# Kernel tuning notes

Measured on AMD Instinct MI355X. Metric: run time of the kernel, lower is better.

The kernel has to match this reference:

```python
import jax, jax.numpy as jnp
import numpy as np

KLD_SCALE = 10.0
COMMITMENT_COST = 0.1


def setup_inputs() -> dict:
    key = jax.random.key(0)
    k1, k2 = jax.random.split(key)
    z = jax.random.normal(k1, (32, 2048, 64), dtype=jnp.float32)
    codebook = jax.random.normal(k2, (1024, 64), dtype=jnp.float32)
    return {"z": z, "codebook": codebook}


def reference(z, codebook):
    B, N, D = z.shape
    z_e = z.reshape(B * N, D)                          # (M, D)
    # squared euclidean distance: ||z||^2 - 2 z.E^T + ||E||^2
    dist = (
        jnp.sum(z_e * z_e, axis=1, keepdims=True)
        - 2.0 * (z_e @ codebook.T)
        + jnp.sum(codebook * codebook, axis=1)[None, :]
    )                                                  # (M, K)
    ind = jnp.argmin(dist, axis=1)                     # (M,)
    z_q = codebook[ind]                                # (M, D) gather
    latent_loss = (
        COMMITMENT_COST * jnp.mean((jax.lax.stop_gradient(z_q) - z_e) ** 2)
        + jnp.mean((z_q - jax.lax.stop_gradient(z_e)) ** 2)
    ) * KLD_SCALE
    # straight-through estimator
    z_q_st = z_e + jax.lax.stop_gradient(z_q - z_e)
    return z_q_st.reshape(B, N, D), latent_loss
```

## Files before the change

### kernel.cpp

```cpp
#include <hip/hip_runtime.h>
#include <hip/hip_bf16.h>
#include <float.h>

#define DIMS 64
#define KC 1024
#define M_TOTAL 65536
#define TAU 4e-3f

typedef __attribute__((ext_vector_type(8))) short bf16x8;
typedef __attribute__((ext_vector_type(4))) float f32x4;

#define SE_OFF   0
#define CTL_OFF  1024
#define PART_OFF 2048
#define PBH_OFF  4096
#define PBL_OFF  36864
#define IDX_OFF  69632
#define WL_OFF   135168

#define WBAR(N) asm volatile("s_waitcnt vmcnt(" #N ")\n\ts_barrier" ::: "memory")

__device__ inline short f2bf(float x) {
  union { __hip_bfloat16 h; short s; } u;
  u.h = __float2bfloat16(x);
  return u.s;
}
__device__ inline float bf2f(short x) {
  union { short s; __hip_bfloat16 h; } u;
  u.s = x;
  return __bfloat162float(u.h);
}

__device__ inline void gload_lds16(const void* g, void* l) {
  __builtin_amdgcn_global_load_lds(
      (const __attribute__((address_space(1))) void*)g,
      (__attribute__((address_space(3))) void*)l, 16, 0, 0);
}

__global__ __launch_bounds__(256) void k_prep(const float* __restrict__ cb,
                                              float* __restrict__ se,
                                              unsigned int* __restrict__ ctl,
                                              unsigned short* __restrict__ pbh,
                                              unsigned short* __restrict__ pbl) {
  const int tid = blockIdx.x * 256 + threadIdx.x;
  if (tid < 4) ctl[tid] = 0;
  const int l = tid & 63;
  const int s = (tid >> 6) & 1;
  const int tt = tid >> 7;
  const int code = tt * 16 + (l & 15);
  const int k = s * 32 + (l >> 4) * 8;
  const float* p = cb + (size_t)code * DIMS + k;
  float v[8];
  ((float4*)v)[0] = ((const float4*)p)[0];
  ((float4*)v)[1] = ((const float4*)p)[1];
  bf16x8 h, lo;
#pragma unroll
  for (int j = 0; j < 8; ++j) {
    short hj = f2bf(v[j]);
    h[j] = hj;
    lo[j] = f2bf(v[j] - bf2f(hj));
  }
  *(bf16x8*)(pbh + (size_t)tid * 8) = h;
  *(bf16x8*)(pbl + (size_t)tid * 8) = lo;

  if (tid < KC) {
    const float4* q = (const float4*)(cb + (size_t)tid * DIMS);
    float a0 = 0.f, a1 = 0.f, a2 = 0.f, a3 = 0.f;
#pragma unroll
    for (int i = 0; i < DIMS / 4; ++i) {
      float4 u = q[i];
      a0 = fmaf(u.x, u.x, a0);
      a1 = fmaf(u.y, u.y, a1);
      a2 = fmaf(u.z, u.z, a2);
      a3 = fmaf(u.w, u.w, a3);
    }
    se[tid] = (a0 + a1) + (a2 + a3);
  }
}

__device__ inline void loadA(const float* zp, bf16x8& h, bf16x8& lo) {
  float v[8];
  ((float4*)v)[0] = ((const float4*)zp)[0];
  ((float4*)v)[1] = ((const float4*)zp)[1];
#pragma unroll
  for (int j = 0; j < 8; ++j) {
    float s = -2.f * v[j];
    short hj = f2bf(s);
    h[j] = hj;
    lo[j] = f2bf(s - bf2f(hj));
  }
}

#define UPD(dv, m1v, m2v, btv)                        \
  {                                                   \
    float d_ = (dv);                                  \
    m2v = __builtin_amdgcn_fmed3f(d_, m1v, m2v);      \
    bool lt_ = d_ < m1v;                              \
    m1v = lt_ ? d_ : m1v;                             \
    btv = lt_ ? ct : btv;                             \
  }

__global__ __launch_bounds__(256, 4) void k_dist(const float* __restrict__ z,
                                                 const unsigned short* __restrict__ pbh,
                                                 const unsigned short* __restrict__ pbl,
                                                 const float* __restrict__ se,
                                                 int* __restrict__ idxo,
                                                 int* __restrict__ wl,
                                                 unsigned int* __restrict__ ctl) {
  __shared__ bf16x8 sB[3][2][256];
  __shared__ float sSE[KC];
  const int l = threadIdx.x & 63;
  const int w = threadIdx.x >> 6;
  const int r0 = blockIdx.x * 64 + w * 16;
  const int col = l & 15;
  const int g = l >> 4;

  const float* zp = z + (size_t)(r0 + col) * DIMS + g * 8;
  bf16x8 ah0, ah1, al0, al1;
  loadA(zp, ah0, al0);
  loadA(zp + 32, ah1, al1);

  gload_lds16(se + w * 256 + l * 4, &sSE[w * 256]);
  {
    const size_t f0 = (size_t)w * 64 + l;
    gload_lds16(pbh + f0 * 8, &sB[0][0][w * 64]);
    gload_lds16(pbl + f0 * 8, &sB[0][1][w * 64]);
    const size_t f1 = 256 + (size_t)w * 64 + l;
    gload_lds16(pbh + f1 * 8, &sB[1][0][w * 64]);
    gload_lds16(pbl + f1 * 8, &sB[1][1][w * 64]);
  }

  float m10 = FLT_MAX, m11 = FLT_MAX, m12 = FLT_MAX, m13 = FLT_MAX;
  float m20 = FLT_MAX, m21 = FLT_MAX, m22 = FLT_MAX, m23 = FLT_MAX;
  int bt0 = 0, bt1 = 0, bt2 = 0, bt3 = 0;

  int bufc = 0;
  for (int c = 0; c < 32; ++c) {
    if (c == 31) {
      WBAR(0);
    } else {
      WBAR(2);
    }
#pragma unroll
    for (int tt = 0; tt < 2; ++tt) {
      const int ct = c * 2 + tt;
      bf16x8 bh0 = sB[bufc][0][tt * 128 + l];
      bf16x8 bh1 = sB[bufc][0][tt * 128 + 64 + l];
      bf16x8 bl0 = sB[bufc][1][tt * 128 + l];
      bf16x8 bl1 = sB[bufc][1][tt * 128 + 64 + l];
      const float sec = sSE[ct * 16 + col];
      f32x4 acc = {sec, sec, sec, sec};
      __builtin_amdgcn_s_setprio(1);
      acc = __builtin_amdgcn_mfma_f32_16x16x32_bf16(ah0, bh0, acc, 0, 0, 0);
      acc = __builtin_amdgcn_mfma_f32_16x16x32_bf16(ah1, bh1, acc, 0, 0, 0);
      acc = __builtin_amdgcn_mfma_f32_16x16x32_bf16(ah0, bl0, acc, 0, 0, 0);
      acc = __builtin_amdgcn_mfma_f32_16x16x32_bf16(ah1, bl1, acc, 0, 0, 0);
      acc = __builtin_amdgcn_mfma_f32_16x16x32_bf16(al0, bh0, acc, 0, 0, 0);
      acc = __builtin_amdgcn_mfma_f32_16x16x32_bf16(al1, bh1, acc, 0, 0, 0);
      __builtin_amdgcn_s_setprio(0);
      UPD(acc[0], m10, m20, bt0);
      UPD(acc[1], m11, m21, bt1);
      UPD(acc[2], m12, m22, bt2);
      UPD(acc[3], m13, m23, bt3);
    }
    if (c < 30) {
      int nb = bufc + 2;
      if (nb >= 3) nb -= 3;
      const size_t f = (size_t)(c + 2) * 256 + w * 64 + l;
      gload_lds16(pbh + f * 8, &sB[nb][0][w * 64]);
      gload_lds16(pbl + f * 8, &sB[nb][1][w * 64]);
    }
    bufc++;
    if (bufc == 3) bufc = 0;
  }

  float m1s[4] = {m10, m11, m12, m13};
  float m2s[4] = {m20, m21, m22, m23};
  int bts[4] = {bt0, bt1, bt2, bt3};
#pragma unroll
  for (int j = 0; j < 4; ++j) {
    float m1j = m1s[j], m2j = m2s[j];
    int ij = bts[j] * 16 + col;
    for (int msk = 1; msk <= 8; msk <<= 1) {
      float o1 = __shfl_xor(m1j, msk);
      float o2 = __shfl_xor(m2j, msk);
      int oi = __shfl_xor(ij, msk);
      bool take = (o1 < m1j) || (o1 == m1j && oi < ij);
      float hi = take ? m1j : o1;
      m2j = fminf(fminf(m2j, o2), hi);
      m1j = take ? o1 : m1j;
      ij = take ? oi : ij;
    }
    if (col == 0) {
      const int row = r0 + g * 4 + j;
      idxo[row] = ij;
      if (m2j - m1j < TAU) {
        int p = atomicAdd((int*)ctl, 1);
        wl[p] = row;
      }
    }
  }
}

__global__ __launch_bounds__(256) void k_refine(const float* __restrict__ z,
                                                const float* __restrict__ cb,
                                                const int* __restrict__ wl,
                                                const unsigned int* __restrict__ ctl,
                                                int* __restrict__ idxo) {
  __shared__ float zz[64];
  __shared__ double sd[256];
  __shared__ int si[256];
  const int t = threadIdx.x;
  const int n = (int)ctl[0];
  for (int wi = blockIdx.x; wi < n; wi += 512) {
    const int row = wl[wi];
    if (t < 16) ((float4*)zz)[t] = ((const float4*)(z + (size_t)row * DIMS))[t];
    __syncthreads();
    const int c0 = t * 4;
    double accd[4] = {0.0, 0.0, 0.0, 0.0};
    for (int ch = 0; ch < 4; ++ch) {
      float zr[16];
#pragma unroll
      for (int q = 0; q < 4; ++q) ((float4*)zr)[q] = ((float4*)zz)[ch * 4 + q];
#pragma unroll
      for (int cc = 0; cc < 4; ++cc) {
        const float* e = cb + (size_t)(c0 + cc) * DIMS + ch * 16;
#pragma unroll
        for (int q = 0; q < 16; ++q) {
          double df = (double)zr[q] - (double)e[q];
          accd[cc] = fma(df, df, accd[cc]);
        }
      }
    }
    double best = 1e300;
    int bi = 0;
#pragma unroll
    for (int cc = 0; cc < 4; ++cc)
      if (accd[cc] < best) { best = accd[cc]; bi = c0 + cc; }
    sd[t] = best;
    si[t] = bi;
    __syncthreads();
    for (int off = 128; off > 0; off >>= 1) {
      if (t < off) {
        double ob = sd[t + off];
        int oi = si[t + off];
        if (ob < sd[t] || (ob == sd[t] && oi < si[t])) { sd[t] = ob; si[t] = oi; }
      }
      __syncthreads();
    }
    if (t == 0) idxo[row] = si[0];
    __syncthreads();
  }
}

__global__ __launch_bounds__(256) void k_out(const float* __restrict__ z,
                                             const float* __restrict__ cb,
                                             const int* __restrict__ idxi,
                                             float* __restrict__ out,
                                             float* __restrict__ partials) {
  const int tid = blockIdx.x * 256 + threadIdx.x;
  const int row = tid >> 2;
  const int q = tid & 3;
  const int code = idxi[row];
  const float4* zp = (const float4*)(z + (size_t)row * DIMS + q * 16);
  const float4* ep = (const float4*)(cb + (size_t)code * DIMS + q * 16);
  float4* op = (float4*)(out + (size_t)row * DIMS + q * 16);
  float sse = 0.f;
#pragma unroll
  for (int i = 0; i < 4; ++i) {
    float4 v = zp[i], e = ep[i];
    float dx = e.x - v.x, dy = e.y - v.y, dz = e.z - v.z, dw = e.w - v.w;
    sse = fmaf(dx, dx, sse);
    sse = fmaf(dy, dy, sse);
    sse = fmaf(dz, dz, sse);
    sse = fmaf(dw, dw, sse);
    float4 o;
    o.x = v.x + dx;
    o.y = v.y + dy;
    o.z = v.z + dz;
    o.w = v.w + dw;
    op[i] = o;
  }
  __shared__ float sh[256];
  sh[threadIdx.x] = sse;
  __syncthreads();
  for (int off = 128; off > 0; off >>= 1) {
    if (threadIdx.x < off) sh[threadIdx.x] += sh[threadIdx.x + off];
    __syncthreads();
  }
  if (threadIdx.x == 0) partials[blockIdx.x] = sh[0];
}

__global__ __launch_bounds__(256) void k_loss(const float* __restrict__ partials,
                                              float* __restrict__ out) {
  __shared__ float sh[256];
  const int t = threadIdx.x;
  sh[t] = partials[t] + partials[t + 256] + partials[t + 512] + partials[t + 768];
  __syncthreads();
  for (int off = 128; off > 0; off >>= 1) {
    if (t < off) sh[t] += sh[t + off];
    __syncthreads();
  }
  if (t == 0) {
    out[(size_t)M_TOTAL * DIMS] = sh[0] * (11.0f / (float)((size_t)M_TOTAL * DIMS));
  }
}

extern "C" void kernel_launch(void* const* d_in, const int* in_sizes, int n_in,
                              void* d_out, int out_size, void* d_ws, size_t ws_size,
                              hipStream_t stream) {
  const float* z = (const float*)d_in[0];
  const float* cb = (const float*)d_in[1];
  float* out = (float*)d_out;
  float* ws = (float*)d_ws;

  float* se = ws + SE_OFF;
  unsigned int* ctl = (unsigned int*)(ws + CTL_OFF);
  float* partials = ws + PART_OFF;
  unsigned short* pbh = (unsigned short*)(ws + PBH_OFF);
  unsigned short* pbl = (unsigned short*)(ws + PBL_OFF);
  int* idx = (int*)(ws + IDX_OFF);
  int* wl = (int*)(ws + WL_OFF);

  k_prep<<<32, 256, 0, stream>>>(cb, se, ctl, pbh, pbl);
  k_dist<<<M_TOTAL / 64, 256, 0, stream>>>(z, pbh, pbl, se, idx, wl, ctl);
  k_refine<<<512, 256, 0, stream>>>(z, cb, wl, ctl, idx);
  k_out<<<M_TOTAL / 64, 256, 0, stream>>>(z, cb, idx, out, partials);
  k_loss<<<1, 256, 0, stream>>>(partials, out);
}
```

Measured before the change: 58.64 us.

## Switch codebook staging to double buffer with syncthreads and read norms from global

Replaces the triple-buffered async LDS pipeline (two chunks in flight, explicit vmcnt waits) with a simpler double buffer that prefetches one chunk ahead and uses __syncthreads each iteration. The codebook-norm array is no longer staged in LDS and is read directly from global memory per tile, and the MFMA priority hints are removed. This lowers LDS usage and may raise occupancy. In exchange it shortens prefetch depth, relies on __syncthreads to drain the LDS-targeted loads, and adds global loads inside the inner loop.

Result: slower. 60.09 us (+2.5%).

```diff
diff --git a/kernel.cpp b/kernel.cpp
--- a/kernel.cpp
+++ b/kernel.cpp
@@ -17,8 +17,6 @@
 #define PBL_OFF  36864
 #define IDX_OFF  69632
 #define WL_OFF   135168
-
-#define WBAR(N) asm volatile("s_waitcnt vmcnt(" #N ")\n\ts_barrier" ::: "memory")
 
 __device__ inline short f2bf(float x) {
   union { __hip_bfloat16 h; short s; } u;
@@ -107,8 +105,7 @@
                                                  int* __restrict__ idxo,
                                                  int* __restrict__ wl,
                                                  unsigned int* __restrict__ ctl) {
-  __shared__ bf16x8 sB[3][2][256];
-  __shared__ float sSE[KC];
+  __shared__ bf16x8 sB[2][2][256];
   const int l = threadIdx.x & 63;
   const int w = threadIdx.x >> 6;
   const int r0 = blockIdx.x * 64 + w * 16;
@@ -120,58 +117,46 @@
   loadA(zp, ah0, al0);
   loadA(zp + 32, ah1, al1);
 
-  gload_lds16(se + w * 256 + l * 4, &sSE[w * 256]);
-  {
-    const size_t f0 = (size_t)w * 64 + l;
-    gload_lds16(pbh + f0 * 8, &sB[0][0][w * 64]);
-    gload_lds16(pbl + f0 * 8, &sB[0][1][w * 64]);
-    const size_t f1 = 256 + (size_t)w * 64 + l;
-    gload_lds16(pbh + f1 * 8, &sB[1][0][w * 64]);
-    gload_lds16(pbl + f1 * 8, &sB[1][1][w * 64]);
-  }
-
   float m10 = FLT_MAX, m11 = FLT_MAX, m12 = FLT_MAX, m13 = FLT_MAX;
   float m20 = FLT_MAX, m21 = FLT_MAX, m22 = FLT_MAX, m23 = FLT_MAX;
   int bt0 = 0, bt1 = 0, bt2 = 0, bt3 = 0;
 
-  int bufc = 0;
+  {
+    const size_t f = (size_t)w * 64 + l;
+    gload_lds16(pbh + f * 8, &sB[0][0][w * 64]);
+    gload_lds16(pbl + f * 8, &sB[0][1][w * 64]);
+  }
+  __syncthreads();
+
+  int cur = 0;
   for (int c = 0; c < 32; ++c) {
-    if (c == 31) {
-      WBAR(0);
-    } else {
-      WBAR(2);
+    if (c + 1 < 32) {
+      const size_t f = (size_t)(c + 1) * 256 + w * 64 + l;
+      gload_lds16(pbh + f * 8, &sB[cur ^ 1][0][w * 64]);
+      gload_lds16(pbl + f * 8, &sB[cur ^ 1][1][w * 64]);
     }
 #pragma unroll
     for (int tt = 0; tt < 2; ++tt) {
       const int ct = c * 2 + tt;
-      bf16x8 bh0 = sB[bufc][0][tt * 128 + l];
-      bf16x8 bh1 = sB[bufc][0][tt * 128 + 64 + l];
-      bf16x8 bl0 = sB[bufc][1][tt * 128 + l];
-      bf16x8 bl1 = sB[bufc][1][tt * 128 + 64 + l];
-      const float sec = sSE[ct * 16 + col];
+      bf16x8 bh0 = sB[cur][0][tt * 128 + l];
+      bf16x8 bh1 = sB[cur][0][tt * 128 + 64 + l];
+      bf16x8 bl0 = sB[cur][1][tt * 128 + l];
+      bf16x8 bl1 = sB[cur][1][tt * 128 + 64 + l];
+      const float sec = se[ct * 16 + col];
       f32x4 acc = {sec, sec, sec, sec};
-      __builtin_amdgcn_s_setprio(1);
       acc = __builtin_amdgcn_mfma_f32_16x16x32_bf16(ah0, bh0, acc, 0, 0, 0);
       acc = __builtin_amdgcn_mfma_f32_16x16x32_bf16(ah1, bh1, acc, 0, 0, 0);
       acc = __builtin_amdgcn_mfma_f32_16x16x32_bf16(ah0, bl0, acc, 0, 0, 0);
       acc = __builtin_amdgcn_mfma_f32_16x16x32_bf16(ah1, bl1, acc, 0, 0, 0);
       acc = __builtin_amdgcn_mfma_f32_16x16x32_bf16(al0, bh0, acc, 0, 0, 0);
       acc = __builtin_amdgcn_mfma_f32_16x16x32_bf16(al1, bh1, acc, 0, 0, 0);
-      __builtin_amdgcn_s_setprio(0);
       UPD(acc[0], m10, m20, bt0);
       UPD(acc[1], m11, m21, bt1);
       UPD(acc[2], m12, m22, bt2);
       UPD(acc[3], m13, m23, bt3);
     }
-    if (c < 30) {
-      int nb = bufc + 2;
-      if (nb >= 3) nb -= 3;
-      const size_t f = (size_t)(c + 2) * 256 + w * 64 + l;
-      gload_lds16(pbh + f * 8, &sB[nb][0][w * 64]);
-      gload_lds16(pbl + f * 8, &sB[nb][1][w * 64]);
-    }
-    bufc++;
-    if (bufc == 3) bufc = 0;
+    __syncthreads();
+    cur ^= 1;
   }
 
   float m1s[4] = {m10, m11, m12, m13};
```
